# Performance work log

Measured on AMD Instinct MI355X. Metric: run time of the kernel, lower is better.

Reference implementation:

```python
import jax, jax.numpy as jnp
import numpy as np

N_NODES = 100000
N_EDGES = 1000000
DIM = 64
N_GRAPHS = 256
OUT_DIM = 10
BN_EPS = 1e-5


def setup_inputs() -> dict:
    key = jax.random.key(0)
    ks = jax.random.split(key, 12)
    s = 0.1  # weight init scale
    x = jax.random.normal(ks[0], (N_NODES, DIM), jnp.float32)
    edge_index = jax.random.randint(ks[1], (2, N_EDGES), 0, N_NODES, dtype=jnp.int32)
    batch = jnp.sort(jax.random.randint(ks[2], (N_NODES,), 0, N_GRAPHS, dtype=jnp.int32))
    w1 = jax.random.normal(ks[3], (3, DIM, DIM), jnp.float32) * s
    b1 = jax.random.normal(ks[4], (3, DIM), jnp.float32) * s
    w2 = jax.random.normal(ks[5], (3, DIM, DIM), jnp.float32) * s
    b2 = jax.random.normal(ks[6], (3, DIM), jnp.float32) * s
    gamma = jax.random.uniform(ks[7], (3, DIM), jnp.float32, 0.5, 1.5)
    beta = jax.random.normal(ks[8], (3, DIM), jnp.float32) * s
    eps_g = jnp.zeros((3,), jnp.float32)  # GIN train_eps, init 0
    lin_w = jax.random.normal(ks[9], (DIM, OUT_DIM), jnp.float32) * s
    lin_b = jax.random.normal(ks[10], (OUT_DIM,), jnp.float32) * s
    return dict(x=x, edge_index=edge_index, batch=batch, w1=w1, b1=b1,
                w2=w2, b2=b2, gamma=gamma, beta=beta, eps_g=eps_g,
                lin_w=lin_w, lin_b=lin_b)


def _gin_layer(x, src, dst, w1, b1, w2, b2, gamma, beta, eps):
    # scatter-add neighbor aggregation: agg[i] = sum_{(j->i) in E} x[j]
    agg = jax.ops.segment_sum(x[src], dst, num_segments=N_NODES)
    h = (1.0 + eps) * x + agg
    h = jax.nn.relu(h @ w1 + b1)
    h = jax.nn.relu(h @ w2 + b2)
    # BatchNorm1d, training-mode batch statistics (biased variance)
    mean = jnp.mean(h, axis=0)
    var = jnp.mean((h - mean) ** 2, axis=0)
    h = (h - mean) * jax.lax.rsqrt(var + BN_EPS) * gamma + beta
    return jax.nn.relu(h)  # outer F.relu(conv(...))


def reference(x, edge_index, batch, w1, b1, w2, b2, gamma, beta, eps_g, lin_w, lin_b):
    src, dst = edge_index[0], edge_index[1]
    for i in range(3):
        x = _gin_layer(x, src, dst, w1[i], b1[i], w2[i], b2[i],
                       gamma[i], beta[i], eps_g[i])
    # global mean pool over graphs
    sums = jax.ops.segment_sum(x, batch, num_segments=N_GRAPHS)
    counts = jax.ops.segment_sum(jnp.ones((x.shape[0],), x.dtype), batch,
                                 num_segments=N_GRAPHS)
    pooled = sums / jnp.maximum(counts, 1.0)[:, None]
    return pooled @ lin_w + lin_b
```

## Files before the change

### kernel.cpp

```cpp
#include <hip/hip_runtime.h>
#include <hip/hip_bf16.h>

#define N_NODES 100000
#define N_EDGES 1000000
#define DIM 64
#define N_GRAPHS 256
#define OUT_DIM 10
#define BN_EPS 1e-5f

#define LAYER_BLOCKS ((N_NODES + 63) / 64)
#define PAD 24
#define SPILL_CAP 8192
#define NPART 8
#define PART_SZ ((N_NODES + NPART - 1) / NPART)

#define EDGE_BLOCKS ((N_EDGES + 255) / 256)
#define XC_BLOCKS ((N_NODES * 16 + 255) / 256)
#define BUILD_BLOCKS (EDGE_BLOCKS + XC_BLOCKS + 6 + 1)

#define BUCK_CAP 131072
#define PLACE_BLOCKS ((BUCK_CAP / 256) * NPART)

#define Z4A 96
#define Z4B 25008
#define ZLIN_BLOCKS ((Z4A + Z4B + 255) / 256)
#define SEG_BLOCKS ((N_NODES + 255) / 256)
#define ZERO_BLOCKS (ZLIN_BLOCKS + SEG_BLOCKS)

typedef __bf16 bf16x8 __attribute__((ext_vector_type(8)));
typedef float f32x4 __attribute__((ext_vector_type(4)));

__device__ __forceinline__ float bfu(unsigned short u) {
    return (float)__builtin_bit_cast(__bf16, u);
}

__global__ __launch_bounds__(256) void zero_kernel(
    uint4* __restrict__ za, uint4* __restrict__ zb,
    const int* __restrict__ batch, int* __restrict__ bstart)
{
    const int bid = blockIdx.x;
    const int tid = threadIdx.x;
    if (bid < ZLIN_BLOCKS) {
        int i = bid * 256 + tid;
        uint4 z = {0u, 0u, 0u, 0u};
        if (i < Z4A) za[i] = z;
        else if (i < Z4A + Z4B) zb[i - Z4A] = z;
    } else {
        int n = (bid - ZLIN_BLOCKS) * 256 + tid;
        if (n < N_NODES) {
            int b = batch[n];
            int bp = (n == 0) ? -1 : batch[n - 1];
            for (int gg = bp + 1; gg <= b; ++gg) bstart[gg] = n;
            if (n == N_NODES - 1)
                for (int gg = b + 1; gg <= N_GRAPHS; ++gg) bstart[gg] = N_NODES;
        }
    }
}

__global__ __launch_bounds__(256) void build_kernel(
    const int* __restrict__ ei, int* __restrict__ pfcnt,
    int2* __restrict__ buck,
    const float* __restrict__ w1, const float* __restrict__ w2,
    __bf16* __restrict__ wf,
    const float4* __restrict__ x0, ushort4* __restrict__ xp4,
    unsigned short* __restrict__ xp_s, unsigned short* __restrict__ xq_s,
    unsigned short* __restrict__ xs_s)
{
    __shared__ int lcnt[NPART];
    __shared__ int gbase[NPART];
    const int bid = blockIdx.x;
    const int tid = threadIdx.x;

    if (bid < EDGE_BLOCKS) {
        const int e = bid * 256 + tid;
        int dstv = -1, srcv = 0;
        if (e < N_EDGES) { dstv = ei[N_EDGES + e]; srcv = ei[e]; }
        int p = (dstv >= 0) ? (dstv / PART_SZ) : -1;

        if (tid < NPART) lcnt[tid] = 0;
        __syncthreads();
        int lbase = 0, rank = 0;
        for (int pp = 0; pp < NPART; ++pp) {
            unsigned long long mask = __ballot(p == pp);
            if (mask == 0ull) continue;
            int leader = __ffsll(mask) - 1;
            int m = __popcll(mask);
            int wb = 0;
            if ((tid & 63) == leader) wb = atomicAdd(&lcnt[pp], m);
            wb = __shfl(wb, leader, 64);
            if (p == pp) {
                lbase = wb;
                rank = __popcll(mask & ((1ull << (unsigned)(tid & 63)) - 1ull));
            }
        }
        __syncthreads();
        if (tid < NPART) gbase[tid] = atomicAdd(&pfcnt[tid], lcnt[tid]);
        __syncthreads();
        if (p >= 0) {
            int slot = gbase[p] + lbase + rank;
            if (slot < BUCK_CAP)
                buck[(size_t)p * BUCK_CAP + slot] = (int2){dstv, srcv};
        }
    } else if (bid < EDGE_BLOCKS + XC_BLOCKS) {
        int t = (bid - EDGE_BLOCKS) * 256 + tid;
        if (t < N_NODES * 16) {
            float4 v = x0[t];
            ushort4 o;
            o.x = __builtin_bit_cast(unsigned short, (__bf16)v.x);
            o.y = __builtin_bit_cast(unsigned short, (__bf16)v.y);
            o.z = __builtin_bit_cast(unsigned short, (__bf16)v.z);
            o.w = __builtin_bit_cast(unsigned short, (__bf16)v.w);
            xp4[t] = o;
        }
    } else if (bid < EDGE_BLOCKS + XC_BLOCKS + 6) {
        int wb = bid - EDGE_BLOCKS - XC_BLOCKS;
        int L = wb >> 1, mat = wb & 1;
        const float* w = (mat ? w2 : w1) + L * 4096;
        __bf16* dst = wf + wb * 8192;
#pragma unroll
        for (int r = 0; r < 2; ++r) {
            int idx = tid + 256 * r;
            int lane = idx & 63;
            int kt = idx >> 6;
            int kstep = kt >> 2, nt = kt & 3;
            int n = nt * 16 + (lane & 15);
            int kbase = kstep * 32 + (lane >> 4) * 8;
#pragma unroll
            for (int j = 0; j < 8; ++j) {
                float v = w[(kbase + j) * 64 + n];
                __bf16 hi = (__bf16)v;
                dst[idx * 8 + j] = hi;
                dst[4096 + idx * 8 + j] = (__bf16)(v - (float)hi);
            }
        }
    } else {
        if (tid < 64) {
            xp_s[tid] = 0;
            xq_s[tid] = 0xFF80;
            xs_s[tid] = 0xFF80;
        }
    }
}

__global__ __launch_bounds__(256) void place_kernel(
    const int* __restrict__ pfcnt, const int2* __restrict__ buck,
    int* __restrict__ deg, int* __restrict__ esrc,
    int* __restrict__ nspill, int* __restrict__ spill)
{
    const int p = blockIdx.x & (NPART - 1);
    const int i = (blockIdx.x >> 3) * 256 + threadIdx.x;
    int n = pfcnt[p];
    n = n < BUCK_CAP ? n : BUCK_CAP;
    if (i >= n) return;
    int2 pr = buck[(size_t)p * BUCK_CAP + i];
    int pos = atomicAdd(&deg[pr.x], 1);
    if (pos < PAD) {
        esrc[pr.x * PAD + pos] = pr.y;
    } else {
        int sp = atomicAdd(nspill, 1);
        if (sp < SPILL_CAP) { spill[2 * sp] = pr.x; spill[2 * sp + 1] = pr.y; }
    }
}

template <bool BN>
__global__ __launch_bounds__(256) void layer_kernel(
    const unsigned short* __restrict__ xb,
    const float* __restrict__ sums_in, const float* __restrict__ gamma,
    const float* __restrict__ beta,
    const int* __restrict__ deg, const int* __restrict__ esrc,
    const int* __restrict__ nspill, const int* __restrict__ spill,
    unsigned short* __restrict__ xbout,
    const __bf16* __restrict__ wf1, const __bf16* __restrict__ wf2,
    const float* __restrict__ b1, const float* __restrict__ b2,
    const float* __restrict__ eps_all, int layer,
    float* __restrict__ sums_out)
{
    __shared__ __attribute__((aligned(16))) unsigned tile[4][16][68];
    __shared__ float bnacc[128];

    const int tid = threadIdx.x;
    const int lane = tid & 63;
    const int wv = tid >> 6;
    const int q = lane >> 4;
    const int r = lane & 15;
    const int node0 = blockIdx.x * 64 + wv * 16;
    const bool active = node0 < N_NODES;

    if (tid < 128) bnacc[tid] = 0.0f;

    float scale = 1.0f, shift = 0.0f;
    if (BN) {
        const float inv_n = 1.0f / (float)N_NODES;
        float mean = sums_in[lane] * inv_n;
        float var = sums_in[64 + lane] * inv_n - mean * mean;
        scale = gamma[lane] * rsqrtf(var + BN_EPS);
        shift = fmaf(-mean, scale, beta[lane]);
    }

    f32x4 acc[4];
    float bs[4], bq[4];
#pragma unroll
    for (int nt = 0; nt < 4; ++nt) {
        acc[nt] = (f32x4){0.f, 0.f, 0.f, 0.f};
        bs[nt] = 0.0f; bq[nt] = 0.0f;
    }

    if (active) {
        const float epsv = 1.0f + eps_all[layer];

        int dvec = 0;
        if (lane < 16) dvec = deg[node0 + lane];
        uint4 nf0, nf1, nf2;
        {
            const uint4* ip = (const uint4*)(esrc + (size_t)node0 * PAD);
            nf0 = ip[0]; nf1 = ip[1]; nf2 = ip[2];
        }
        for (int i = 0; i < 16; ++i) {
            const uint4 c0 = nf0, c1 = nf1, c2 = nf2;
            if (i < 15) {
                const uint4* ip = (const uint4*)(esrc + (size_t)(node0 + i + 1) * PAD);
                nf0 = ip[0]; nf1 = ip[1]; nf2 = ip[2];
            }
            const int n = node0 + i;
            const int dfull = __builtin_amdgcn_readlane(dvec, i);
            const int d = min(dfull, PAD);

            float xv = bfu(xb[(size_t)n * 64 + lane]);
            if (BN) xv = fmaxf(fmaf(xv, scale, shift), 0.0f);
            float hval = epsv * xv;

            {
                unsigned idx[12] = {c0.x, c0.y, c0.z, c0.w, c1.x, c1.y,
                                    c1.z, c1.w, c2.x, c2.y, c2.z, c2.w};
                unsigned short u[12];
#pragma unroll
                for (int j = 0; j < 12; ++j) {
                    unsigned s = idx[j];
                    s = (s < (unsigned)N_NODES) ? s : (unsigned)N_NODES;
                    u[j] = xb[(size_t)s * 64 + lane];
                }
#pragma unroll
                for (int j = 0; j < 12; ++j) {
                    float t = bfu(u[j]);
                    if (BN) t = fmaxf(fmaf(t, scale, shift), 0.0f);
                    hval += t;
                }
            }
            if (d > 12) {
                const int* ep = esrc + (size_t)n * PAD + 12;
                unsigned short u[12];
#pragma unroll
                for (int j = 0; j < 12; ++j) {
                    unsigned s = (unsigned)ep[j];
                    s = (s < (unsigned)N_NODES) ? s : (unsigned)N_NODES;
                    u[j] = xb[(size_t)s * 64 + lane];
                }
#pragma unroll
                for (int j = 0; j < 12; ++j) {
                    float t = bfu(u[j]);
                    if (BN) t = fmaxf(fmaf(t, scale, shift), 0.0f);
                    hval += t;
                }
            }
            if (dfull > PAD) {
                int ns = min(*nspill, SPILL_CAP);
                for (int e = 0; e < ns; ++e) {
                    if (spill[2 * e] == n) {
                        float t = bfu(xb[(size_t)spill[2 * e + 1] * 64 + lane]);
                        if (BN) t = fmaxf(fmaf(t, scale, shift), 0.0f);
                        hval += t;
                    }
                }
            }
            __bf16 hi = (__bf16)hval;
            __bf16 lo = (__bf16)(hval - (float)hi);
            tile[wv][i][lane] = ((unsigned)__builtin_bit_cast(unsigned short, hi) << 16)
                              | (unsigned)__builtin_bit_cast(unsigned short, lo);
        }

        uint4 f0 = *(const uint4*)&tile[wv][r][q * 8];
        uint4 f1 = *(const uint4*)&tile[wv][r][q * 8 + 4];
        uint4 f2 = *(const uint4*)&tile[wv][r][32 + q * 8];
        uint4 f3 = *(const uint4*)&tile[wv][r][32 + q * 8 + 4];
#pragma unroll
        for (int kstep = 0; kstep < 2; ++kstep) {
            uint4 p0 = kstep ? f2 : f0;
            uint4 p1 = kstep ? f3 : f1;
            unsigned pk[8] = {p0.x, p0.y, p0.z, p0.w, p1.x, p1.y, p1.z, p1.w};
            bf16x8 ahi, alo;
#pragma unroll
            for (int j = 0; j < 8; ++j) {
                ahi[j] = __builtin_bit_cast(__bf16, (unsigned short)(pk[j] >> 16));
                alo[j] = __builtin_bit_cast(__bf16, (unsigned short)(pk[j] & 0xffffu));
            }
#pragma unroll
            for (int nt = 0; nt < 4; ++nt) {
                const __bf16* bp = wf1 + ((kstep * 4 + nt) * 64 + lane) * 8;
                bf16x8 bhi = *(const bf16x8*)bp;
                bf16x8 blo = *(const bf16x8*)(bp + 4096);
                acc[nt] = __builtin_amdgcn_mfma_f32_16x16x32_bf16(ahi, bhi, acc[nt], 0, 0, 0);
                acc[nt] = __builtin_amdgcn_mfma_f32_16x16x32_bf16(alo, bhi, acc[nt], 0, 0, 0);
                acc[nt] = __builtin_amdgcn_mfma_f32_16x16x32_bf16(ahi, blo, acc[nt], 0, 0, 0);
            }
        }
#pragma unroll
        for (int nt = 0; nt < 4; ++nt) {
            float b1v = b1[nt * 16 + r];
#pragma unroll
            for (int reg = 0; reg < 4; ++reg) {
                float v = fmaxf(acc[nt][reg] + b1v, 0.0f);
                __bf16 hi = (__bf16)v;
                __bf16 lo = (__bf16)(v - (float)hi);
                unsigned pk = ((unsigned)__builtin_bit_cast(unsigned short, hi) << 16)
                            | (unsigned)__builtin_bit_cast(unsigned short, lo);
                tile[wv][q * 4 + reg][nt * 16 + r] = pk;
            }
            acc[nt] = (f32x4){0.f, 0.f, 0.f, 0.f};
        }
#pragma unroll
        for (int kstep = 0; kstep < 2; ++kstep) {
            uint4 p0 = *(const uint4*)&tile[wv][r][kstep * 32 + q * 8];
            uint4 p1 = *(const uint4*)&tile[wv][r][kstep * 32 + q * 8 + 4];
            unsigned pk[8] = {p0.x, p0.y, p0.z, p0.w, p1.x, p1.y, p1.z, p1.w};
            bf16x8 ahi, alo;
#pragma unroll
            for (int j = 0; j < 8; ++j) {
                ahi[j] = __builtin_bit_cast(__bf16, (unsigned short)(pk[j] >> 16));
                alo[j] = __builtin_bit_cast(__bf16, (unsigned short)(pk[j] & 0xffffu));
            }
#pragma unroll
            for (int nt = 0; nt < 4; ++nt) {
                const __bf16* bp = wf2 + ((kstep * 4 + nt) * 64 + lane) * 8;
                bf16x8 bhi = *(const bf16x8*)bp;
                bf16x8 blo = *(const bf16x8*)(bp + 4096);
                acc[nt] = __builtin_amdgcn_mfma_f32_16x16x32_bf16(ahi, bhi, acc[nt], 0, 0, 0);
                acc[nt] = __builtin_amdgcn_mfma_f32_16x16x32_bf16(alo, bhi, acc[nt], 0, 0, 0);
                acc[nt] = __builtin_amdgcn_mfma_f32_16x16x32_bf16(ahi, blo, acc[nt], 0, 0, 0);
            }
        }
#pragma unroll
        for (int nt = 0; nt < 4; ++nt) {
            float b2v = b2[nt * 16 + r];
#pragma unroll
            for (int reg = 0; reg < 4; ++reg) {
                float v = fmaxf(acc[nt][reg] + b2v, 0.0f);
                size_t oi = (size_t)(node0 + q * 4 + reg) * 64 + nt * 16 + r;
                xbout[oi] = __builtin_bit_cast(unsigned short, (__bf16)v);
                bs[nt] += v;
                bq[nt] = fmaf(v, v, bq[nt]);
            }
        }
    }
    __syncthreads();
#pragma unroll
    for (int nt = 0; nt < 4; ++nt) {
        float s = bs[nt];
        s += __shfl_xor(s, 16);
        s += __shfl_xor(s, 32);
        float ss = bq[nt];
        ss += __shfl_xor(ss, 16);
        ss += __shfl_xor(ss, 32);
        if (q == 0) {
            atomicAdd(&bnacc[nt * 16 + r], s);
            atomicAdd(&bnacc[64 + nt * 16 + r], ss);
        }
    }
    __syncthreads();
    if (tid < 128) unsafeAtomicAdd(&sums_out[tid], bnacc[tid]);
}

__global__ __launch_bounds__(1024) void head_kernel(
    const unsigned short* __restrict__ h2b, const float* __restrict__ sums,
    const float* __restrict__ gamma, const float* __restrict__ beta,
    const int* __restrict__ bstart, const float* __restrict__ lin_w,
    const float* __restrict__ lin_b, float* __restrict__ out)
{
    __shared__ float red[16][64];
    __shared__ float pooled_s[64];
    const int g = blockIdx.x;
    const int tid = threadIdx.x;
    const int lane = tid & 63;
    const int wv = tid >> 6;
    const int lo = bstart[g];
    const int hi = bstart[g + 1];

    const float inv_n = 1.0f / (float)N_NODES;
    float mean = sums[lane] * inv_n;
    float var = sums[64 + lane] * inv_n - mean * mean;
    const float scale = gamma[lane] * rsqrtf(var + BN_EPS);
    const float shift = fmaf(-mean, scale, beta[lane]);

    float acc = 0.0f;
    for (int n = lo + wv; n < hi; n += 16) {
        float v = bfu(h2b[(size_t)n * 64 + lane]);
        acc += fmaxf(fmaf(v, scale, shift), 0.0f);
    }
    red[wv][lane] = acc;
    __syncthreads();
    if (wv == 0) {
        float s = 0.0f;
#pragma unroll
        for (int w = 0; w < 16; ++w) s += red[w][lane];
        float c = fmaxf((float)(hi - lo), 1.0f);
        pooled_s[lane] = s / c;
    }
    __syncthreads();
    if (tid < OUT_DIM) {
        float a2 = lin_b[tid];
#pragma unroll
        for (int d = 0; d < 64; ++d)
            a2 = fmaf(pooled_s[d], lin_w[d * OUT_DIM + tid], a2);
        out[g * OUT_DIM + tid] = a2;
    }
}

extern "C" void kernel_launch(void* const* d_in, const int* in_sizes, int n_in,
                              void* d_out, int out_size, void* d_ws, size_t ws_size,
                              hipStream_t stream)
{
    const float* x0    = (const float*)d_in[0];
    const int*   ei    = (const int*)d_in[1];
    const int*   batch = (const int*)d_in[2];
    const float* w1    = (const float*)d_in[3];
    const float* b1    = (const float*)d_in[4];
    const float* w2    = (const float*)d_in[5];
    const float* b2    = (const float*)d_in[6];
    const float* gamma = (const float*)d_in[7];
    const float* beta  = (const float*)d_in[8];
    const float* eps_g = (const float*)d_in[9];
    const float* lin_w = (const float*)d_in[10];
    const float* lin_b = (const float*)d_in[11];
    float* out = (float*)d_out;

    float* ws   = (float*)d_ws;
    float* SUMS = ws;
    float* POOL = SUMS + 384;
    float* CNT  = POOL + N_GRAPHS * 64;
    int*   DEG    = (int*)(CNT + N_GRAPHS);
    int*   NSPILL = DEG + N_NODES;
    int*   PFCNT  = NSPILL + 16;
    __bf16* WF  = (__bf16*)(PFCNT + 16);
    int*   SPILL  = (int*)(WF + 6 * 8192);
    int*   ESRC   = SPILL + 2 * SPILL_CAP;
    unsigned short* XP = (unsigned short*)(ESRC + (size_t)N_NODES * PAD);
    unsigned short* XQ = XP + (size_t)(N_NODES + 1) * 64;
    unsigned short* XS = XQ + (size_t)(N_NODES + 1) * 64;
    unsigned short* XR = XS + (size_t)(N_NODES + 1) * 64;

    int*  BSTART = (int*)POOL;
    int2* BUCK   = (int2*)XR;

    zero_kernel<<<ZERO_BLOCKS, 256, 0, stream>>>(
        (uint4*)SUMS, (uint4*)DEG, batch, BSTART);

    build_kernel<<<BUILD_BLOCKS, 256, 0, stream>>>(
        ei, PFCNT, BUCK, w1, w2, WF, (const float4*)x0, (ushort4*)XP,
        XP + (size_t)N_NODES * 64, XQ + (size_t)N_NODES * 64,
        XS + (size_t)N_NODES * 64);

    place_kernel<<<PLACE_BLOCKS, 256, 0, stream>>>(
        PFCNT, BUCK, DEG, ESRC, NSPILL, SPILL);

    layer_kernel<false><<<LAYER_BLOCKS, 256, 0, stream>>>(
        XP, nullptr, nullptr, nullptr, DEG, ESRC, NSPILL, SPILL, XQ,
        WF, WF + 8192, b1, b2, eps_g, 0, SUMS);

    layer_kernel<true><<<LAYER_BLOCKS, 256, 0, stream>>>(
        XQ, SUMS, gamma, beta, DEG, ESRC, NSPILL, SPILL, XS,
        WF + 16384, WF + 24576, b1 + 64, b2 + 64, eps_g, 1, SUMS + 128);

    layer_kernel<true><<<LAYER_BLOCKS, 256, 0, stream>>>(
        XS, SUMS + 128, gamma + 64, beta + 64, DEG, ESRC, NSPILL, SPILL, XR,
        WF + 32768, WF + 40960, b1 + 128, b2 + 128, eps_g, 2, SUMS + 256);

    head_kernel<<<N_GRAPHS, 1024, 0, stream>>>(
        XR, SUMS + 256, gamma + 128, beta + 128, BSTART, lin_w, lin_b, out);
}
```

Baseline: 381.4 us.

## Replace two-pass bucketed edge placement with single partition-filtered fill kernel

Removes the bucket staging pass (ballot ranking into per-partition buckets, then a separate place kernel) and instead launches NPART blocks per edge chunk, where each block keeps only edges whose destination falls in its partition and does the degree atomic and ELL write directly. This drops one kernel launch and the bucket write/read traffic. In exchange, the destination indices are read eight times and most threads exit early, while partition locality of the atomics is kept through block ordering.

```diff
diff --git a/kernel.cpp b/kernel.cpp
--- a/kernel.cpp
+++ b/kernel.cpp
@@ -14,12 +14,9 @@
 #define NPART 8
 #define PART_SZ ((N_NODES + NPART - 1) / NPART)
 
-#define EDGE_BLOCKS ((N_EDGES + 255) / 256)
+#define FILL_BLOCKS (((N_EDGES + 255) / 256) * NPART)
 #define XC_BLOCKS ((N_NODES * 16 + 255) / 256)
-#define BUILD_BLOCKS (EDGE_BLOCKS + XC_BLOCKS + 6 + 1)
-
-#define BUCK_CAP 131072
-#define PLACE_BLOCKS ((BUCK_CAP / 256) * NPART)
+#define FF_BLOCKS (FILL_BLOCKS + XC_BLOCKS + 6 + 1)
 
 #define Z4A 96
 #define Z4B 25008
@@ -57,52 +54,35 @@
     }
 }
 
-__global__ __launch_bounds__(256) void build_kernel(
-    const int* __restrict__ ei, int* __restrict__ pfcnt,
-    int2* __restrict__ buck,
+__global__ __launch_bounds__(256) void fill_kernel(
+    const int* __restrict__ ei, int* __restrict__ deg,
+    int* __restrict__ esrc, int* __restrict__ nspill, int* __restrict__ spill,
     const float* __restrict__ w1, const float* __restrict__ w2,
     __bf16* __restrict__ wf,
     const float4* __restrict__ x0, ushort4* __restrict__ xp4,
     unsigned short* __restrict__ xp_s, unsigned short* __restrict__ xq_s,
     unsigned short* __restrict__ xs_s)
 {
-    __shared__ int lcnt[NPART];
-    __shared__ int gbase[NPART];
     const int bid = blockIdx.x;
     const int tid = threadIdx.x;
 
-    if (bid < EDGE_BLOCKS) {
-        const int e = bid * 256 + tid;
-        int dstv = -1, srcv = 0;
-        if (e < N_EDGES) { dstv = ei[N_EDGES + e]; srcv = ei[e]; }
-        int p = (dstv >= 0) ? (dstv / PART_SZ) : -1;
-
-        if (tid < NPART) lcnt[tid] = 0;
-        __syncthreads();
-        int lbase = 0, rank = 0;
-        for (int pp = 0; pp < NPART; ++pp) {
-            unsigned long long mask = __ballot(p == pp);
-            if (mask == 0ull) continue;
-            int leader = __ffsll(mask) - 1;
-            int m = __popcll(mask);
-            int wb = 0;
-            if ((tid & 63) == leader) wb = atomicAdd(&lcnt[pp], m);
-            wb = __shfl(wb, leader, 64);
-            if (p == pp) {
-                lbase = wb;
-                rank = __popcll(mask & ((1ull << (unsigned)(tid & 63)) - 1ull));
-            }
-        }
-        __syncthreads();
-        if (tid < NPART) gbase[tid] = atomicAdd(&pfcnt[tid], lcnt[tid]);
-        __syncthreads();
-        if (p >= 0) {
-            int slot = gbase[p] + lbase + rank;
-            if (slot < BUCK_CAP)
-                buck[(size_t)p * BUCK_CAP + slot] = (int2){dstv, srcv};
-        }
-    } else if (bid < EDGE_BLOCKS + XC_BLOCKS) {
-        int t = (bid - EDGE_BLOCKS) * 256 + tid;
+    if (bid < FILL_BLOCKS) {
+        const int part = bid & (NPART - 1);
+        const int e = (bid >> 3) * 256 + tid;
+        if (e >= N_EDGES) return;
+        int dst = ei[N_EDGES + e];
+        int lo = part * PART_SZ;
+        if (dst < lo || dst >= lo + PART_SZ) return;
+        int src = ei[e];
+        int pos = atomicAdd(&deg[dst], 1);
+        if (pos < PAD) {
+            esrc[dst * PAD + pos] = src;
+        } else {
+            int sp = atomicAdd(nspill, 1);
+            if (sp < SPILL_CAP) { spill[2 * sp] = dst; spill[2 * sp + 1] = src; }
+        }
+    } else if (bid < FILL_BLOCKS + XC_BLOCKS) {
+        int t = (bid - FILL_BLOCKS) * 256 + tid;
         if (t < N_NODES * 16) {
             float4 v = x0[t];
             ushort4 o;
@@ -112,8 +92,8 @@
             o.w = __builtin_bit_cast(unsigned short, (__bf16)v.w);
             xp4[t] = o;
         }
-    } else if (bid < EDGE_BLOCKS + XC_BLOCKS + 6) {
-        int wb = bid - EDGE_BLOCKS - XC_BLOCKS;
+    } else if (bid < FILL_BLOCKS + XC_BLOCKS + 6) {
+        int wb = bid - FILL_BLOCKS - XC_BLOCKS;
         int L = wb >> 1, mat = wb & 1;
         const float* w = (mat ? w2 : w1) + L * 4096;
         __bf16* dst = wf + wb * 8192;
@@ -139,26 +119,6 @@
             xq_s[tid] = 0xFF80;
             xs_s[tid] = 0xFF80;
         }
-    }
-}
-
-__global__ __launch_bounds__(256) void place_kernel(
-    const int* __restrict__ pfcnt, const int2* __restrict__ buck,
-    int* __restrict__ deg, int* __restrict__ esrc,
-    int* __restrict__ nspill, int* __restrict__ spill)
-{
-    const int p = blockIdx.x & (NPART - 1);
-    const int i = (blockIdx.x >> 3) * 256 + threadIdx.x;
-    int n = pfcnt[p];
-    n = n < BUCK_CAP ? n : BUCK_CAP;
-    if (i >= n) return;
-    int2 pr = buck[(size_t)p * BUCK_CAP + i];
-    int pos = atomicAdd(&deg[pr.x], 1);
-    if (pos < PAD) {
-        esrc[pr.x * PAD + pos] = pr.y;
-    } else {
-        int sp = atomicAdd(nspill, 1);
-        if (sp < SPILL_CAP) { spill[2 * sp] = pr.x; spill[2 * sp + 1] = pr.y; }
     }
 }
 
@@ -447,19 +407,16 @@
     unsigned short* XS = XQ + (size_t)(N_NODES + 1) * 64;
     unsigned short* XR = XS + (size_t)(N_NODES + 1) * 64;
 
-    int*  BSTART = (int*)POOL;
-    int2* BUCK   = (int2*)XR;
+    int* BSTART = (int*)POOL;
 
     zero_kernel<<<ZERO_BLOCKS, 256, 0, stream>>>(
         (uint4*)SUMS, (uint4*)DEG, batch, BSTART);
 
-    build_kernel<<<BUILD_BLOCKS, 256, 0, stream>>>(
-        ei, PFCNT, BUCK, w1, w2, WF, (const float4*)x0, (ushort4*)XP,
+    fill_kernel<<<FF_BLOCKS, 256, 0, stream>>>(
+        ei, DEG, ESRC, NSPILL, SPILL,
+        w1, w2, WF, (const float4*)x0, (ushort4*)XP,
         XP + (size_t)N_NODES * 64, XQ + (size_t)N_NODES * 64,
         XS + (size_t)N_NODES * 64);
-
-    place_kernel<<<PLACE_BLOCKS, 256, 0, stream>>>(
-        PFCNT, BUCK, DEG, ESRC, NSPILL, SPILL);
 
     layer_kernel<false><<<LAYER_BLOCKS, 256, 0, stream>>>(
         XP, nullptr, nullptr, nullptr, DEG, ESRC, NSPILL, SPILL, XQ,
```

After: 334.1 us, median of 2. 1.14x faster.
